# Optimization experiments

Hardware: AMD Instinct MI355X
Metric: run time of the kernel (lower is better)

Reference implementation:

```python
import jax, jax.numpy as jnp
import numpy as np

N_NODES = 100000


def gcn_conv(x, W, b, src, dst, n):
    # PyG GCNConv: add self-loops, symmetric deg^-1/2 normalization,
    # transform then gather/scatter-add aggregate.
    loop = jnp.arange(n, dtype=src.dtype)
    s = jnp.concatenate([src, loop])
    d = jnp.concatenate([dst, loop])
    deg = jax.ops.segment_sum(jnp.ones_like(d, dtype=x.dtype), d, num_segments=n)
    dinv = jnp.where(deg > 0, 1.0 / jnp.sqrt(deg), 0.0)
    norm = dinv[s] * dinv[d]                      # [E+N]
    h = x @ W                                     # [N, out]
    msgs = h[s] * norm[:, None]                   # gather + scale
    out = jax.ops.segment_sum(msgs, d, num_segments=n)  # scatter-add
    return out + b


def setup_inputs() -> dict:
    key = jax.random.key(0)
    k1, k2, k3, k4 = jax.random.split(key, 4)
    F_in, H, D = 128, 16, 128
    x = jax.random.normal(k1, (N_NODES, F_in), dtype=jnp.float32)
    edge_index = jax.random.randint(k2, (2, 1600000), 0, N_NODES, dtype=jnp.int64)
    W1 = jax.random.normal(k3, (F_in, H), dtype=jnp.float32) / np.sqrt(F_in)
    b1 = jnp.zeros((H,), dtype=jnp.float32)
    W2 = jax.random.normal(k4, (H, D), dtype=jnp.float32) / np.sqrt(H)
    b2 = jnp.zeros((D,), dtype=jnp.float32)
    return {"x": x, "edge_index": edge_index, "W1": W1, "b1": b1, "W2": W2, "b2": b2}


def reference(x, edge_index, W1, b1, W2, b2):
    src, dst = edge_index[0], edge_index[1]
    n = x.shape[0]
    h = jax.nn.relu(gcn_conv(x, W1, b1, src, dst, n))
    out = jax.nn.relu(gcn_conv(h, W2, b2, src, dst, n))
    return out
```

## Files before the change

kernel.cpp:

```cpp
#include <hip/hip_runtime.h>
#include <hip/hip_fp16.h>
#include <stdint.h>

#define F_IN  128
#define HID   16
#define F_OUT 128
#define NBK   512
#define NBLK  512
#define BCAP  4096
#define CHUNK_MAX 4096
#define GT2_NODES 128
#define T1N   64
#define AGP   24

typedef _Float16 f16;
typedef f16 f16x4 __attribute__((ext_vector_type(4)));
typedef f16 f16x8 __attribute__((ext_vector_type(8)));
typedef float f32x4 __attribute__((ext_vector_type(4)));

__device__ __forceinline__ int bucket_of(int d, int N) {
    return (int)(((long long)d * NBK) / N);
}
__device__ __forceinline__ int bucket_lo(int b, int N) {
    return (int)(((long long)b * N + NBK - 1) / NBK);
}

__global__ void __launch_bounds__(256) k_partf(
        const int* __restrict__ ei, int* __restrict__ bcur,
        uint32_t* __restrict__ pairs, int E, int N) {
    __shared__ int lh[NBK], lofs[NBK], lcur[NBK], gbase[NBK], lnlo[NBK];
    __shared__ int loff[256];
    __shared__ uint32_t spairs[CHUNK_MAX];
    __shared__ uint16_t sbkt[CHUNK_MAX];

    int blk = blockIdx.x, t = threadIdx.x;
    int Cr = (E + NBLK - 1) / NBLK;
    int C  = (Cr + 15) & ~15;
    int e0 = blk * C; if (e0 > E) e0 = E;
    int e1 = e0 + C;  if (e1 > E) e1 = E;
    int ecnt = e1 - e0;

    for (int i = t; i < NBK; i += 256) { lh[i] = 0; lnlo[i] = bucket_lo(i, N); }
    __syncthreads();

    int4 es4[4], ed4[4];
    bool evec = ((E & 3) == 0);
#pragma unroll
    for (int j = 0; j < 4; ++j) {
        int e = e0 + (j * 256 + t) * 4;
        if (evec && e + 4 <= e1) {
            es4[j] = *(const int4*)(ei + e);
            ed4[j] = *(const int4*)(ei + E + e);
        } else {
            int* s = (int*)&es4[j];
            int* d = (int*)&ed4[j];
#pragma unroll
            for (int q = 0; q < 4; ++q) {
                int ee = e + q;
                bool ok = (ee < e1);
                s[q] = ok ? ei[ee] : -1;
                d[q] = ok ? ei[E + ee] : 0;
            }
        }
    }
    const int* esv = (const int*)es4;
    const int* edv = (const int*)ed4;
    int eb[16];
#pragma unroll
    for (int k = 0; k < 16; ++k) {
        if (esv[k] >= 0) {
            eb[k] = bucket_of(edv[k], N);
            atomicAdd(&lh[eb[k]], 1);
        } else eb[k] = -1;
    }
    __syncthreads();

    int a0 = lh[2 * t], a1 = lh[2 * t + 1];
    int s2 = a0 + a1;
    loff[t] = s2;
    __syncthreads();
    for (int o = 1; o < 256; o <<= 1) {
        int a = (t >= o) ? loff[t - o] : 0;
        __syncthreads();
        loff[t] += a;
        __syncthreads();
    }
    int excl = loff[t] - s2;
    lofs[2 * t]     = excl;
    lofs[2 * t + 1] = excl + a0;
    lcur[2 * t]     = excl;
    lcur[2 * t + 1] = excl + a0;
    __syncthreads();

    for (int w = 0; w < NBK; w += 256) {
        int i = (t + w + blk) & (NBK - 1);
        int h = lh[i];
        gbase[i] = h ? atomicAdd(&bcur[i], h) : 0;
    }

#pragma unroll
    for (int k = 0; k < 16; ++k) {
        if (eb[k] >= 0) {
            int b = eb[k];
            int idx = atomicAdd(&lcur[b], 1);
            spairs[idx] = ((uint32_t)esv[k] << 10) | (uint32_t)(edv[k] - lnlo[b]);
            sbkt[idx]   = (uint16_t)b;
        }
    }
    __syncthreads();

    for (int i = t; i < ecnt; i += 256) {
        int b = sbkt[i];
        int pos = gbase[b] + (i - lofs[b]);
        if (pos < BCAP)
            pairs[(size_t)b * BCAP + pos] = spairs[i];
    }
}

__global__ void __launch_bounds__(256) k_csr2(
        const uint32_t* __restrict__ pairs, const int* __restrict__ bcur,
        int2* __restrict__ meta, float* __restrict__ dinv,
        int* __restrict__ srcs, int N) {
    __shared__ uint32_t sp[BCAP];
    __shared__ int lcnt[256];
    __shared__ int loff[256];
    __shared__ int lcur[256];
    int b = blockIdx.x, t = threadIdx.x;
    int base = b * BCAP;
    int ec = bcur[b]; if (ec > BCAP) ec = BCAP;
    int nlo = bucket_lo(b, N);
    int nhi = bucket_lo(b + 1, N); if (nhi > N) nhi = N;
    int nn = nhi - nlo;
    lcnt[t] = 0;
    __syncthreads();
    int ec4 = (ec + 3) >> 2;
    for (int i = t; i < ec4; i += 256) {
        uint4 v = *(const uint4*)(pairs + base + i * 4);
        *(uint4*)&sp[i * 4] = v;
        int lim = ec - i * 4;
        if (lim > 0) atomicAdd(&lcnt[v.x & 1023u], 1);
        if (lim > 1) atomicAdd(&lcnt[v.y & 1023u], 1);
        if (lim > 2) atomicAdd(&lcnt[v.z & 1023u], 1);
        if (lim > 3) atomicAdd(&lcnt[v.w & 1023u], 1);
    }
    __syncthreads();
    int v = lcnt[t];
    int pv = (v + 3) & ~3;
    loff[t] = pv;
    __syncthreads();
    for (int o = 1; o < 256; o <<= 1) {
        int a = (t >= o) ? loff[t - o] : 0;
        __syncthreads();
        loff[t] += a;
        __syncthreads();
    }
    if (t < nn) {
        int gs = base + (loff[t] - pv);
        meta[nlo + t] = make_int2(gs, v);
        dinv[nlo + t] = rsqrtf((float)(v + 1));
        lcur[t]       = gs;
    }
    __syncthreads();
    for (int e = t; e < ec; e += 256) {
        uint32_t p = sp[e];
        int pos = atomicAdd(&lcur[p & 1023u], 1);
        srcs[pos] = (int)(p >> 10);
    }
}

__global__ void __launch_bounds__(256) k_transform1(
        const float* __restrict__ x, const float* __restrict__ W1,
        const float* __restrict__ dinv, __half* __restrict__ g1, int n) {
    __shared__ float sX[T1N * 132];
    __shared__ float sW[128 * 17 + 4];
    int t = threadIdx.x;
    int node0 = blockIdx.x * T1N;
    for (int i = t; i < F_IN * HID; i += 256)
        sW[(i >> 4) * 17 + (i & 15)] = W1[i];
    {
        const float4* xg = (const float4*)(x + (size_t)node0 * F_IN);
        int nrem = n - node0;
#pragma unroll
        for (int j = 0; j < 8; ++j) {
            int idx = t + j * 256;
            int r = idx >> 5, c4 = idx & 31;
            float4 v = make_float4(0.f, 0.f, 0.f, 0.f);
            if (r < nrem) v = xg[idx];
            *(float4*)&sX[r * 132 + c4 * 4] = v;
        }
    }
    __syncthreads();
    int lane = t & 63, wave = t >> 6;
    int mcol = lane & 15, kg = lane >> 4;
    f32x4 acc = {0.f, 0.f, 0.f, 0.f};
#pragma unroll
    for (int ks = 0; ks < 4; ++ks) {
        int k0 = ks * 32 + kg * 8;
        const float* xp = &sX[(wave * 16 + mcol) * 132 + k0];
        float4 v0 = *(const float4*)xp;
        float4 v1 = *(const float4*)(xp + 4);
        float va[8] = {v0.x, v0.y, v0.z, v0.w, v1.x, v1.y, v1.z, v1.w};
        f16x8 ah, al;
#pragma unroll
        for (int q = 0; q < 8; ++q) {
            f16 h = (f16)va[q];
            ah[q] = h;
            al[q] = (f16)(va[q] - (float)h);
        }
        const float* wp = &sW[k0 * 17 + mcol];
        f16x8 bh, bl;
#pragma unroll
        for (int q = 0; q < 8; ++q) {
            float wv = wp[q * 17];
            f16 h = (f16)wv;
            bh[q] = h;
            bl[q] = (f16)(wv - (float)h);
        }
        acc = __builtin_amdgcn_mfma_f32_16x16x32_f16(ah, bh, acc, 0, 0, 0);
        acc = __builtin_amdgcn_mfma_f32_16x16x32_f16(al, bh, acc, 0, 0, 0);
        acc = __builtin_amdgcn_mfma_f32_16x16x32_f16(ah, bl, acc, 0, 0, 0);
    }
#pragma unroll
    for (int r = 0; r < 4; ++r) {
        int node = node0 + wave * 16 + kg * 4 + r;
        if (node < n) {
            float di = dinv[node];
            g1[(size_t)node * HID + mcol] = __float2half(di * acc[r]);
        }
    }
}

__device__ __forceinline__ void add_h8(float* __restrict__ acc, const __half* __restrict__ ptr) {
    uint4 u = *(const uint4*)ptr;
    const __half2* h = (const __half2*)&u;
#pragma unroll
    for (int q = 0; q < 4; ++q) {
        float2 f = __half22float2(h[q]);
        acc[2 * q]     += f.x;
        acc[2 * q + 1] += f.y;
    }
}

__device__ __forceinline__ void gather_acc(
        float* __restrict__ acc, int node, int p,
        const __half* __restrict__ g, const int* __restrict__ srcs,
        int rs, int deg) {
    {
        uint4 u = *(const uint4*)(g + (size_t)node * HID + p * 8);
        const __half2* h = (const __half2*)&u;
#pragma unroll
        for (int q = 0; q < 4; ++q) {
            float2 f = __half22float2(h[q]);
            acc[2 * q] = f.x; acc[2 * q + 1] = f.y;
        }
    }
    int j = 0;
    for (; j + 8 <= deg; j += 8) {
        int4 ia = *(const int4*)(srcs + rs + j);
        int4 ib = *(const int4*)(srcs + rs + j + 4);
        add_h8(acc, g + (size_t)ia.x * HID + p * 8);
        add_h8(acc, g + (size_t)ia.y * HID + p * 8);
        add_h8(acc, g + (size_t)ia.z * HID + p * 8);
        add_h8(acc, g + (size_t)ia.w * HID + p * 8);
        add_h8(acc, g + (size_t)ib.x * HID + p * 8);
        add_h8(acc, g + (size_t)ib.y * HID + p * 8);
        add_h8(acc, g + (size_t)ib.z * HID + p * 8);
        add_h8(acc, g + (size_t)ib.w * HID + p * 8);
    }
    if (j + 4 <= deg) {
        int4 ia = *(const int4*)(srcs + rs + j);
        add_h8(acc, g + (size_t)ia.x * HID + p * 8);
        add_h8(acc, g + (size_t)ia.y * HID + p * 8);
        add_h8(acc, g + (size_t)ia.z * HID + p * 8);
        add_h8(acc, g + (size_t)ia.w * HID + p * 8);
        j += 4;
    }
    for (; j < deg; ++j)
        add_h8(acc, g + (size_t)srcs[rs + j] * HID + p * 8);
}

__global__ void __launch_bounds__(256) k_gather1(
        const __half* __restrict__ g, const int* __restrict__ srcs,
        const int2* __restrict__ meta, const float* __restrict__ dinv,
        const float* __restrict__ b1, __half* __restrict__ outb, int n) {
    int tt = blockIdx.x * 256 + threadIdx.x;
    int node = tt >> 1;
    int p = tt & 1;
    if (node >= n) return;
    int2 m = meta[node];
    float acc[8];
    gather_acc(acc, node, p, g, srcs, m.x, m.y);
    float di = dinv[node];
#pragma unroll
    for (int i = 0; i < 8; ++i)
        acc[i] = di * fmaxf(di * acc[i] + b1[p * 8 + i], 0.0f);
    uint4 o;
    __half2* oh = (__half2*)&o;
#pragma unroll
    for (int q = 0; q < 4; ++q)
        oh[q] = __floats2half2_rn(acc[2 * q], acc[2 * q + 1]);
    *(uint4*)(outb + (size_t)node * HID + p * 8) = o;
}

__global__ void __launch_bounds__(256) k_gather_t2(
        const __half* __restrict__ g, const int* __restrict__ srcs,
        const int2* __restrict__ meta, const float* __restrict__ dinv,
        const float* __restrict__ W2, const float* __restrict__ b2,
        float* __restrict__ out, int n) {
    __shared__ __half sAgg[GT2_NODES * AGP];
    __shared__ float  sdv[GT2_NODES];
    int t = threadIdx.x;
    int node0 = blockIdx.x * GT2_NODES;

    {
        int nl = t >> 1, p = t & 1;
        int node = node0 + nl;
        if (node < n) {
            if (p == 0) sdv[nl] = dinv[node];
            int2 m = meta[node];
            float acc[8];
            gather_acc(acc, node, p, g, srcs, m.x, m.y);
            uint4 o;
            __half2* oh = (__half2*)&o;
#pragma unroll
            for (int q = 0; q < 4; ++q)
                oh[q] = __floats2half2_rn(acc[2 * q], acc[2 * q + 1]);
            *(uint4*)&sAgg[nl * AGP + p * 8] = o;
        }
    }
    __syncthreads();

    int lane = t & 63, wave = t >> 6;
    int fcol = lane & 15, kg = lane >> 4;
    int k0 = kg * 4;
    f16x4 bh[8], bl[8];
    float b2v[8];
#pragma unroll
    for (int nt = 0; nt < 8; ++nt) {
        b2v[nt] = b2[nt * 16 + fcol];
#pragma unroll
        for (int j = 0; j < 4; ++j) {
            float wv = W2[(k0 + j) * F_OUT + nt * 16 + fcol];
            f16 h = (f16)wv;
            bh[nt][j] = h;
            bl[nt][j] = (f16)(wv - (float)h);
        }
    }
    const f16* sA = (const f16*)sAgg;
    f16x4 aA = *(const f16x4*)&sA[(wave * 32 + fcol) * AGP + k0];
    f16x4 aB = *(const f16x4*)&sA[(wave * 32 + 16 + fcol) * AGP + k0];
    f32x4 zero = {0.f, 0.f, 0.f, 0.f};
    f32x4 acc[2][8];
#pragma unroll
    for (int mt = 0; mt < 2; ++mt)
#pragma unroll
        for (int nt = 0; nt < 8; ++nt)
            acc[mt][nt] = zero;
#pragma unroll
    for (int nt = 0; nt < 8; ++nt) {
        acc[0][nt] = __builtin_amdgcn_mfma_f32_16x16x16f16(aA, bh[nt], acc[0][nt], 0, 0, 0);
        acc[0][nt] = __builtin_amdgcn_mfma_f32_16x16x16f16(aA, bl[nt], acc[0][nt], 0, 0, 0);
        acc[1][nt] = __builtin_amdgcn_mfma_f32_16x16x16f16(aB, bh[nt], acc[1][nt], 0, 0, 0);
        acc[1][nt] = __builtin_amdgcn_mfma_f32_16x16x16f16(aB, bl[nt], acc[1][nt], 0, 0, 0);
    }
#pragma unroll
    for (int mt = 0; mt < 2; ++mt) {
#pragma unroll
        for (int r = 0; r < 4; ++r) {
            int ln = wave * 32 + mt * 16 + kg * 4 + r;
            int node = node0 + ln;
            if (node < n) {
                float dv = sdv[ln];
#pragma unroll
                for (int nt = 0; nt < 8; ++nt)
                    out[(size_t)node * F_OUT + nt * 16 + fcol] =
                        fmaxf(dv * acc[mt][nt][r] + b2v[nt], 0.f);
            }
        }
    }
}

extern "C" void kernel_launch(void* const* d_in, const int* in_sizes, int n_in,
                              void* d_out, int out_size, void* d_ws, size_t ws_size,
                              hipStream_t stream) {
    const float* x  = (const float*)d_in[0];
    const int*   ei = (const int*)d_in[1];
    const float* W1 = (const float*)d_in[2];
    const float* b1 = (const float*)d_in[3];
    const float* W2 = (const float*)d_in[4];
    const float* b2 = (const float*)d_in[5];
    float* out = (float*)d_out;

    const int N = in_sizes[0] / F_IN;
    const int E = in_sizes[1] / 2;

    float* dinv      = (float*)d_ws;
    int2*  meta      = (int2*)(dinv + N);
    int*   bcur      = (int*)(meta + N);
    int*   srcs      = bcur + NBK;
    uint32_t* pairs  = (uint32_t*)(srcs + (size_t)NBK * BCAP);
    __half* bufA     = (__half*)(pairs + (size_t)NBK * BCAP);
    __half* bufB     = bufA + (size_t)N * HID;

    hipMemsetAsync(bcur, 0, NBK * sizeof(int), stream);
    k_partf<<<NBLK, 256, 0, stream>>>(ei, bcur, pairs, E, N);
    k_csr2 <<<NBK, 256, 0, stream>>>(pairs, bcur, meta, dinv, srcs, N);
    k_transform1<<<(N + T1N - 1) / T1N, 256, 0, stream>>>(x, W1, dinv, bufA, N);
    k_gather1<<<((size_t)N * 2 + 255) / 256, 256, 0, stream>>>(
        bufA, srcs, meta, dinv, b1, bufB, N);
    k_gather_t2<<<(N + GT2_NODES - 1) / GT2_NODES, 256, 0, stream>>>(
        bufB, srcs, meta, dinv, W2, b2, out, N);
}
```

Before: 196.9 us.

## Double partition buckets and load transform1 inputs directly from global

The edge partition now uses twice as many buckets and blocks, with half the per-block chunk and bucket capacity, so each block handles 8 edges per thread and the scan covers 4 buckets per thread. Separately, transform1 no longer stages x through shared memory. Each lane reads its row straight from global memory, and W1 is pre-split into fp16 high and low halves in transposed shared arrays that are loaded as vectors. This reduces shared memory use and per-element conversion work, but the bucket capacity of 2048 leaves less headroom against overflow, and the global reads from x are strided across rows.

After: 198.3 us. No clear change (+0.7%).

```diff
diff --git a/kernel.cpp b/kernel.cpp
--- a/kernel.cpp
+++ b/kernel.cpp
@@ -5,13 +5,14 @@
 #define F_IN  128
 #define HID   16
 #define F_OUT 128
-#define NBK   512
-#define NBLK  512
-#define BCAP  4096
-#define CHUNK_MAX 4096
+#define NBK   1024
+#define NBLK  1024
+#define BCAP  2048
+#define CHUNK_MAX 2048
 #define GT2_NODES 128
 #define T1N   64
 #define AGP   24
+#define WP    136
 
 typedef _Float16 f16;
 typedef f16 f16x4 __attribute__((ext_vector_type(4)));
@@ -43,10 +44,10 @@
     for (int i = t; i < NBK; i += 256) { lh[i] = 0; lnlo[i] = bucket_lo(i, N); }
     __syncthreads();
 
-    int4 es4[4], ed4[4];
+    int4 es4[2], ed4[2];
     bool evec = ((E & 3) == 0);
 #pragma unroll
-    for (int j = 0; j < 4; ++j) {
+    for (int j = 0; j < 2; ++j) {
         int e = e0 + (j * 256 + t) * 4;
         if (evec && e + 4 <= e1) {
             es4[j] = *(const int4*)(ei + e);
@@ -65,9 +66,9 @@
     }
     const int* esv = (const int*)es4;
     const int* edv = (const int*)ed4;
-    int eb[16];
-#pragma unroll
-    for (int k = 0; k < 16; ++k) {
+    int eb[8];
+#pragma unroll
+    for (int k = 0; k < 8; ++k) {
         if (esv[k] >= 0) {
             eb[k] = bucket_of(edv[k], N);
             atomicAdd(&lh[eb[k]], 1);
@@ -75,9 +76,9 @@
     }
     __syncthreads();
 
-    int a0 = lh[2 * t], a1 = lh[2 * t + 1];
-    int s2 = a0 + a1;
-    loff[t] = s2;
+    int a0 = lh[4 * t], a1 = lh[4 * t + 1], a2 = lh[4 * t + 2], a3 = lh[4 * t + 3];
+    int s4 = a0 + a1 + a2 + a3;
+    loff[t] = s4;
     __syncthreads();
     for (int o = 1; o < 256; o <<= 1) {
         int a = (t >= o) ? loff[t - o] : 0;
@@ -85,11 +86,15 @@
         loff[t] += a;
         __syncthreads();
     }
-    int excl = loff[t] - s2;
-    lofs[2 * t]     = excl;
-    lofs[2 * t + 1] = excl + a0;
-    lcur[2 * t]     = excl;
-    lcur[2 * t + 1] = excl + a0;
+    int excl = loff[t] - s4;
+    lofs[4 * t]     = excl;
+    lofs[4 * t + 1] = excl + a0;
+    lofs[4 * t + 2] = excl + a0 + a1;
+    lofs[4 * t + 3] = excl + a0 + a1 + a2;
+    lcur[4 * t]     = lofs[4 * t];
+    lcur[4 * t + 1] = lofs[4 * t + 1];
+    lcur[4 * t + 2] = lofs[4 * t + 2];
+    lcur[4 * t + 3] = lofs[4 * t + 3];
     __syncthreads();
 
     for (int w = 0; w < NBK; w += 256) {
@@ -99,7 +104,7 @@
     }
 
 #pragma unroll
-    for (int k = 0; k < 16; ++k) {
+    for (int k = 0; k < 8; ++k) {
         if (eb[k] >= 0) {
             int b = eb[k];
             int idx = atomicAdd(&lcur[b], 1);
@@ -171,34 +176,29 @@
 __global__ void __launch_bounds__(256) k_transform1(
         const float* __restrict__ x, const float* __restrict__ W1,
         const float* __restrict__ dinv, __half* __restrict__ g1, int n) {
-    __shared__ float sX[T1N * 132];
-    __shared__ float sW[128 * 17 + 4];
+    __shared__ __align__(16) f16 sWh[HID * WP];
+    __shared__ __align__(16) f16 sWl[HID * WP];
     int t = threadIdx.x;
     int node0 = blockIdx.x * T1N;
-    for (int i = t; i < F_IN * HID; i += 256)
-        sW[(i >> 4) * 17 + (i & 15)] = W1[i];
-    {
-        const float4* xg = (const float4*)(x + (size_t)node0 * F_IN);
-        int nrem = n - node0;
-#pragma unroll
-        for (int j = 0; j < 8; ++j) {
-            int idx = t + j * 256;
-            int r = idx >> 5, c4 = idx & 31;
-            float4 v = make_float4(0.f, 0.f, 0.f, 0.f);
-            if (r < nrem) v = xg[idx];
-            *(float4*)&sX[r * 132 + c4 * 4] = v;
-        }
+    for (int i = t; i < F_IN * HID; i += 256) {
+        int k = i >> 4, f = i & 15;
+        float wv = W1[i];
+        f16 h = (f16)wv;
+        sWh[f * WP + k] = h;
+        sWl[f * WP + k] = (f16)(wv - (float)h);
     }
     __syncthreads();
     int lane = t & 63, wave = t >> 6;
     int mcol = lane & 15, kg = lane >> 4;
+    int nrow = node0 + wave * 16 + mcol;
+    int crow = nrow < n ? nrow : (n - 1);
+    const float* xr = x + (size_t)crow * F_IN;
     f32x4 acc = {0.f, 0.f, 0.f, 0.f};
 #pragma unroll
     for (int ks = 0; ks < 4; ++ks) {
         int k0 = ks * 32 + kg * 8;
-        const float* xp = &sX[(wave * 16 + mcol) * 132 + k0];
-        float4 v0 = *(const float4*)xp;
-        float4 v1 = *(const float4*)(xp + 4);
+        float4 v0 = *(const float4*)(xr + k0);
+        float4 v1 = *(const float4*)(xr + k0 + 4);
         float va[8] = {v0.x, v0.y, v0.z, v0.w, v1.x, v1.y, v1.z, v1.w};
         f16x8 ah, al;
 #pragma unroll
@@ -207,15 +207,8 @@
             ah[q] = h;
             al[q] = (f16)(va[q] - (float)h);
         }
-        const float* wp = &sW[k0 * 17 + mcol];
-        f16x8 bh, bl;
-#pragma unroll
-        for (int q = 0; q < 8; ++q) {
-            float wv = wp[q * 17];
-            f16 h = (f16)wv;
-            bh[q] = h;
-            bl[q] = (f16)(wv - (float)h);
-        }
+        f16x8 bh = *(const f16x8*)&sWh[mcol * WP + k0];
+        f16x8 bl = *(const f16x8*)&sWl[mcol * WP + k0];
         acc = __builtin_amdgcn_mfma_f32_16x16x32_f16(ah, bh, acc, 0, 0, 0);
         acc = __builtin_amdgcn_mfma_f32_16x16x32_f16(al, bh, acc, 0, 0, 0);
         acc = __builtin_amdgcn_mfma_f32_16x16x32_f16(ah, bl, acc, 0, 0, 0);
```
